# Kernel optimization log

Hardware: AMD Instinct MI355X
Metric: run time of the kernel (lower is better)

Reference implementation:

```python
import jax, jax.numpy as jnp
import numpy as np

B, S, H = 2, 2048, 2048
NH, NKV, HD = 32, 8, 64          # num_heads, num_kv_heads, head_dim
G = NH // NKV                     # GQA group size
NEG = -1e9


def setup_inputs() -> dict:
    key = jax.random.key(0)
    ks = jax.random.split(key, 8)
    x = jax.random.normal(ks[0], (B, S, H), dtype=jnp.float32)
    # real RoPE frequencies: theta = 10000 ** (-2i/hd)
    inv_freq = 1.0 / (10000.0 ** (np.arange(0, HD, 2, dtype=np.float32) / HD))
    angles = np.arange(S, dtype=np.float32)[:, None] * inv_freq[None, :]  # [S, HD//2]
    freqs_cos = jnp.asarray(np.cos(angles))
    freqs_sin = jnp.asarray(np.sin(angles))
    # additive causal mask [S, S]
    mask = jnp.where(jnp.tril(jnp.ones((S, S), dtype=bool)), 0.0, NEG).astype(jnp.float32)
    sc = 0.02
    Wq = jax.random.normal(ks[1], (NH * HD, H), dtype=jnp.float32) * sc
    bq = jax.random.normal(ks[2], (NH * HD,), dtype=jnp.float32) * sc
    Wk = jax.random.normal(ks[3], (NKV * HD, H), dtype=jnp.float32) * sc
    bk = jax.random.normal(ks[4], (NKV * HD,), dtype=jnp.float32) * sc
    Wv = jax.random.normal(ks[5], (NKV * HD, H), dtype=jnp.float32) * sc
    bv = jax.random.normal(ks[6], (NKV * HD,), dtype=jnp.float32) * sc
    Wo = jax.random.normal(ks[7], (H, NH * HD), dtype=jnp.float32) * sc
    return {"x": x, "freqs_cos": freqs_cos, "freqs_sin": freqs_sin, "mask": mask,
            "Wq": Wq, "bq": bq, "Wk": Wk, "bk": bk, "Wv": Wv, "bv": bv, "Wo": Wo}


def _rotate_half(t):
    h = t.shape[-1] // 2
    return jnp.concatenate([-t[..., h:], t[..., :h]], axis=-1)


def reference(x, freqs_cos, freqs_sin, mask, Wq, bq, Wk, bk, Wv, bv, Wo):
    b, s, _ = x.shape
    q = (x @ Wq.T + bq).reshape(b, s, NH, HD)
    k = (x @ Wk.T + bk).reshape(b, s, NKV, HD)
    v = (x @ Wv.T + bv).reshape(b, s, NKV, HD)
    # RoPE (rotate_half style): cos/sin duplicated along last dim -> [1, s, 1, HD]
    cos = jnp.concatenate([freqs_cos, freqs_cos], axis=-1)[None, :, None, :]
    sin = jnp.concatenate([freqs_sin, freqs_sin], axis=-1)[None, :, None, :]
    q = q * cos + _rotate_half(q) * sin
    k = k * cos + _rotate_half(k) * sin
    # GQA: view q as [b, s, NKV, G, HD]; avoids repeat_interleave of K/V (same math)
    q5 = q.reshape(b, s, NKV, G, HD)
    scores = jnp.einsum('bqhgd,bkhd->bhgqk', q5, k) / jnp.sqrt(jnp.float32(HD))
    scores = scores + mask  # broadcast [s, s] over [b, h, g, s, s]
    p = jax.nn.softmax(scores.astype(jnp.float32), axis=-1).astype(q.dtype)
    out = jnp.einsum('bhgqk,bkhd->bqhgd', p, v).reshape(b, s, NH * HD)
    return out @ Wo.T
```

## Files before the change

kernel.cpp:

```cpp
#include <hip/hip_runtime.h>
#include <hip/hip_bf16.h>
#include <cstddef>
#include <cstdint>

#define B_   2
#define S_   2048
#define H_   2048
#define NH_  32
#define NKV_ 8
#define HD_  64

typedef __attribute__((ext_vector_type(8))) short short8;
typedef __attribute__((ext_vector_type(4))) float v4f;
typedef __attribute__((ext_vector_type(16))) float v16f;

#define MAXC 48.0f
#define QSCALE 0.18033688011112042f

__device__ __forceinline__ unsigned short f2b(float f) {
    unsigned int u = __float_as_uint(f);
    u += 0x7FFFu + ((u >> 16) & 1u);
    return (unsigned short)(u >> 16);
}
__device__ __forceinline__ unsigned int pkbf(float a, float b) {
    __hip_bfloat162 h = __float22bfloat162_rn(float2{a, b});
    return *(unsigned int*)&h;
}
__device__ __forceinline__ v4f mfma16(short8 a, short8 b, v4f c) {
    return __builtin_amdgcn_mfma_f32_16x16x32_bf16(a, b, c, 0, 0, 0);
}
__device__ __forceinline__ v16f mfma32(short8 a, short8 b, v16f c) {
    return __builtin_amdgcn_mfma_f32_32x32x16_bf16(a, b, c, 0, 0, 0);
}
__device__ __forceinline__ void gll16(void* lds, const void* g) {
    __builtin_amdgcn_global_load_lds(
        (const __attribute__((address_space(1))) unsigned int*)g,
        (__attribute__((address_space(3))) unsigned int*)lds, 16, 0, 0);
}

__global__ __launch_bounds__(256) void convert_all(
    const float* __restrict__ x, const float* __restrict__ wq,
    const float* __restrict__ wk, const float* __restrict__ wv,
    const float* __restrict__ wo,
    unsigned short* __restrict__ xb, unsigned short* __restrict__ wqb,
    unsigned short* __restrict__ wkb, unsigned short* __restrict__ wvb,
    unsigned short* __restrict__ wob)
{
    size_t i = ((size_t)blockIdx.x * 256 + threadIdx.x) * 4;
    const float* src; unsigned short* dst; size_t off;
    if (i < 8388608)       { src = x;  dst = xb;  off = i; }
    else if (i < 12582912) { src = wq; dst = wqb; off = i - 8388608; }
    else if (i < 13631488) { src = wk; dst = wkb; off = i - 12582912; }
    else if (i < 14680064) { src = wv; dst = wvb; off = i - 13631488; }
    else                   { src = wo; dst = wob; off = i - 14680064; }
    float4 v = *(const float4*)(src + off);
    ushort4 o;
    o.x = f2b(v.x); o.y = f2b(v.y); o.z = f2b(v.z); o.w = f2b(v.w);
    *(ushort4*)(dst + off) = o;
}

__global__ __launch_bounds__(256) void qkv_gemm(
    const unsigned short* __restrict__ xb,
    const unsigned short* __restrict__ wqb, const unsigned short* __restrict__ wkb,
    const unsigned short* __restrict__ wvb,
    const float* __restrict__ bq, const float* __restrict__ bk,
    const float* __restrict__ bv,
    const float* __restrict__ fc, const float* __restrict__ fs,
    unsigned short* __restrict__ Qb, unsigned short* __restrict__ Kb,
    unsigned short* __restrict__ Vt)
{
    __shared__ unsigned short As[128 * 64];
    __shared__ unsigned short Bs[128 * 64];
    const int tid = threadIdx.x;
    const int lane = tid & 63, w = tid >> 6;
    const int tx = lane & 15, quad = lane >> 4;
    const int bx = blockIdx.x, by = blockIdx.y;

    const unsigned short *Ap, *Bp;
    int mode, aBase, bBase;
    if (bx < 16)      { mode = 0; Ap = xb;  Bp = wqb; aBase = by * 128; bBase = bx * 128; }
    else if (bx < 20) { mode = 1; Ap = xb;  Bp = wkb; aBase = by * 128; bBase = (bx - 16) * 128; }
    else              { mode = 2; Ap = wvb; Bp = xb;  aBase = (bx - 20) * 128; bBase = by * 128; }

    const int wm = (w >> 1) * 64, wn = (w & 1) * 64;
    v4f acc[4][4];
#pragma unroll
    for (int i = 0; i < 4; ++i)
#pragma unroll
        for (int j = 0; j < 4; ++j) acc[i][j] = (v4f)0.f;

    const int r8 = lane >> 3, gc = (lane & 7) ^ r8;
    const unsigned short* ga = &Ap[(size_t)(aBase + w * 32 + r8) * 2048 + gc * 8];
    const unsigned short* gb = &Bp[(size_t)(bBase + w * 32 + r8) * 2048 + gc * 8];

    const int t7 = tx & 7;
    int slA[2], slB[2];
#pragma unroll
    for (int kk = 0; kk < 2; ++kk) { slA[kk] = ((kk * 4 + quad) ^ t7) * 8; slB[kk] = slA[kk]; }

    for (int k0 = 0; k0 < 2048; k0 += 64) {
        __syncthreads();
#pragma unroll
        for (int i = 0; i < 4; ++i) {
            gll16(&As[(w * 32 + i * 8) * 64], ga + (size_t)(i * 8) * 2048 + k0);
            gll16(&Bs[(w * 32 + i * 8) * 64], gb + (size_t)(i * 8) * 2048 + k0);
        }
        __syncthreads();
#pragma unroll
        for (int kk = 0; kk < 2; ++kk) {
            short8 af[4], bf[4];
#pragma unroll
            for (int mt = 0; mt < 4; ++mt)
                af[mt] = *(const short8*)&As[(wm + mt * 16 + tx) * 64 + slA[kk]];
#pragma unroll
            for (int nt = 0; nt < 4; ++nt)
                bf[nt] = *(const short8*)&Bs[(wn + nt * 16 + tx) * 64 + slB[kk]];
#pragma unroll
            for (int mt = 0; mt < 4; ++mt)
#pragma unroll
                for (int nt = 0; nt < 4; ++nt)
                    acc[mt][nt] = mfma16(af[mt], bf[nt], acc[mt][nt]);
        }
    }

    if (mode <= 1) {
        unsigned short* Cout = mode ? Kb : Qb;
        const float* bias    = mode ? bk : bq;
        const int ldN        = mode ? 512 : 2048;
        const float scq      = mode ? 1.0f : QSCALE;
        float bx0 = bias[bBase + wn +  0 + tx];
        float bx1 = bias[bBase + wn + 16 + tx];
        float bx2 = bias[bBase + wn + 32 + tx];
        float bx3 = bias[bBase + wn + 48 + tx];
#pragma unroll
        for (int mt = 0; mt < 4; ++mt)
#pragma unroll
            for (int rg = 0; rg < 4; ++rg) {
                int m = aBase + wm + mt * 16 + quad * 4 + rg;
                int s = m & (S_ - 1);
                float c0 = fc[s * 32 + tx],      c1 = fc[s * 32 + 16 + tx];
                float s0 = fs[s * 32 + tx],      s1 = fs[s * 32 + 16 + tx];
                float q0 = acc[mt][0][rg] + bx0, q1 = acc[mt][1][rg] + bx1;
                float q2 = acc[mt][2][rg] + bx2, q3 = acc[mt][3][rg] + bx3;
                size_t base = (size_t)m * ldN + bBase + wn + tx;
                Cout[base]      = f2b((q0 * c0 - q2 * s0) * scq);
                Cout[base + 16] = f2b((q1 * c1 - q3 * s1) * scq);
                Cout[base + 32] = f2b((q2 * c0 + q0 * s0) * scq);
                Cout[base + 48] = f2b((q3 * c1 + q1 * s1) * scq);
            }
    } else {
#pragma unroll
        for (int mt = 0; mt < 4; ++mt)
#pragma unroll
            for (int rg = 0; rg < 4; ++rg) {
                int d = aBase + wm + mt * 16 + quad * 4 + rg;
                float bvv = bv[d];
                size_t base = (size_t)d * 4096 + bBase + wn + tx;
#pragma unroll
                for (int nt = 0; nt < 4; ++nt)
                    Vt[base + nt * 16] = f2b(acc[mt][nt][rg] + bvv);
            }
    }
}

__global__ __launch_bounds__(256) void out_gemm(
    const unsigned short* __restrict__ Ab, const unsigned short* __restrict__ Bw,
    float* __restrict__ C)
{
    __shared__ unsigned short As[128 * 64];
    __shared__ unsigned short Bs[128 * 64];
    const int tid = threadIdx.x;
    const int lane = tid & 63, w = tid >> 6;
    const int tx = lane & 15, quad = lane >> 4;
    const int bm = blockIdx.y * 128, bn = blockIdx.x * 128;
    const int wm = (w >> 1) * 64, wn = (w & 1) * 64;

    v4f acc[4][4];
#pragma unroll
    for (int i = 0; i < 4; ++i)
#pragma unroll
        for (int j = 0; j < 4; ++j) acc[i][j] = (v4f)0.f;

    const int r8 = lane >> 3, gc = (lane & 7) ^ r8;
    const unsigned short* ga = &Ab[(size_t)(bm + w * 32 + r8) * 2048 + gc * 8];
    const unsigned short* gb = &Bw[(size_t)(bn + w * 32 + r8) * 2048 + gc * 8];
    const int t7 = tx & 7;
    int sl[2];
#pragma unroll
    for (int kk = 0; kk < 2; ++kk) sl[kk] = ((kk * 4 + quad) ^ t7) * 8;

    for (int k0 = 0; k0 < 2048; k0 += 64) {
        __syncthreads();
#pragma unroll
        for (int i = 0; i < 4; ++i) {
            gll16(&As[(w * 32 + i * 8) * 64], ga + (size_t)(i * 8) * 2048 + k0);
            gll16(&Bs[(w * 32 + i * 8) * 64], gb + (size_t)(i * 8) * 2048 + k0);
        }
        __syncthreads();
#pragma unroll
        for (int kk = 0; kk < 2; ++kk) {
            short8 af[4], bf[4];
#pragma unroll
            for (int mt = 0; mt < 4; ++mt)
                af[mt] = *(const short8*)&As[(wm + mt * 16 + tx) * 64 + sl[kk]];
#pragma unroll
            for (int nt = 0; nt < 4; ++nt)
                bf[nt] = *(const short8*)&Bs[(wn + nt * 16 + tx) * 64 + sl[kk]];
#pragma unroll
            for (int mt = 0; mt < 4; ++mt)
#pragma unroll
                for (int nt = 0; nt < 4; ++nt)
                    acc[mt][nt] = mfma16(af[mt], bf[nt], acc[mt][nt]);
        }
    }
#pragma unroll
    for (int mt = 0; mt < 4; ++mt)
#pragma unroll
        for (int nt = 0; nt < 4; ++nt)
#pragma unroll
            for (int rg = 0; rg < 4; ++rg) {
                int m = bm + wm + mt * 16 + quad * 4 + rg;
                C[(size_t)m * 2048 + bn + wn + nt * 16 + tx] = acc[mt][nt][rg];
            }
}

__global__ __launch_bounds__(256) void attn_mfma(
    const unsigned short* __restrict__ Q, const unsigned short* __restrict__ K,
    const unsigned short* __restrict__ Vt, unsigned short* __restrict__ O)
{
    __shared__ __align__(16) unsigned short Ks[64 * 72];
    __shared__ __align__(16) unsigned short Vs[64 * 72];
    const int tid = threadIdx.x;
    const int lane = tid & 63, wq = tid >> 6;
    const int l32 = lane & 31, half = lane >> 5;
    const int p = blockIdx.x, h = blockIdx.y, b = blockIdx.z;
    const int kvh = h >> 2;
    const int qtw = (wq < 2) ? p : (31 - p);
    const int kt_hi = 31 - p;

    const int qrow = qtw * 64 + (wq & 1) * 32 + l32;
    const unsigned short* Qr = &Q[(((size_t)b * S_ + qrow) * NH_ + h) * HD_];
    short8 qf[4];
#pragma unroll
    for (int s = 0; s < 4; ++s)
        qf[s] = *(const short8*)(Qr + s * 16 + half * 8);

    float l = 0.f;
    v16f o0 = (v16f)0.f, o1 = (v16f)0.f;

    for (int kt = 0; kt <= kt_hi; ++kt) {
        __syncthreads();
#pragma unroll
        for (int i = 0; i < 2; ++i) {
            int e = tid + i * 256;
            int row = e >> 3, c8 = (e & 7) * 8;
            *(uint4*)&Ks[row * 72 + c8] =
                *(const uint4*)&K[(((size_t)b * S_ + kt * 64 + row) * NKV_ + kvh) * HD_ + c8];
            *(uint4*)&Vs[row * 72 + c8] =
                *(const uint4*)&Vt[(size_t)(kvh * 64 + row) * 4096 + b * 2048 + kt * 64 + c8];
        }
        __syncthreads();
        if (kt > qtw) continue;
        const bool diag = (kt == qtw);
        const int tpart = diag ? (wq & 1) : 2;

        for (int t = 0; t < 2; ++t) {
            if (diag && t > tpart) break;
            const int kb = (t * 32 + l32) * 72 + half * 8;
            v16f st = (v16f)(-MAXC);
            st = mfma32(*(const short8*)&Ks[kb],      qf[0], st);
            st = mfma32(*(const short8*)&Ks[kb + 16], qf[1], st);
            st = mfma32(*(const short8*)&Ks[kb + 32], qf[2], st);
            st = mfma32(*(const short8*)&Ks[kb + 48], qf[3], st);
            const bool part = diag && (t == tpart);
            float pv[16];
#pragma unroll
            for (int r = 0; r < 16; ++r) {
                int krow = (r & 3) + 8 * (r >> 2) + 4 * half;
                bool msk = part && (krow > l32);
                pv[r] = msk ? 0.f : exp2f(st[r]);
                l += pv[r];
            }
            unsigned int u[8];
#pragma unroll
            for (int g = 0; g < 4; ++g) {
                u[2 * g]     = pkbf(pv[4 * g],     pv[4 * g + 1]);
                u[2 * g + 1] = pkbf(pv[4 * g + 2], pv[4 * g + 3]);
            }
#pragma unroll
            for (int sg = 0; sg < 2; ++sg) {
                unsigned int a0 = u[4 * sg], a1 = u[4 * sg + 1];
                unsigned int b0 = u[4 * sg + 2], b1 = u[4 * sg + 3];
                unsigned int s0 = __shfl_xor((int)a0, 32);
                unsigned int s1 = __shfl_xor((int)a1, 32);
                unsigned int s2 = __shfl_xor((int)b0, 32);
                unsigned int s3 = __shfl_xor((int)b1, 32);
                uint4 fw;
                fw.x = half ? s2 : a0;
                fw.y = half ? s3 : a1;
                fw.z = half ? b0 : s0;
                fw.w = half ? b1 : s1;
                short8 pf = *(short8*)&fw;
                const int vo = (2 * t + sg) * 16 + half * 8;
                o0 = mfma32(*(const short8*)&Vs[l32 * 72 + vo],        pf, o0);
                o1 = mfma32(*(const short8*)&Vs[(32 + l32) * 72 + vo], pf, o1);
            }
        }
    }

    l += __shfl_xor(l, 32);
    float inv = 1.f / l;
    int qg = qtw * 64 + (wq & 1) * 32 + l32;
    unsigned short* orow = &O[((size_t)b * S_ + qg) * (NH_ * HD_) + h * HD_];
#pragma unroll
    for (int td = 0; td < 2; ++td) {
        const v16f& oo = td ? o1 : o0;
#pragma unroll
        for (int g = 0; g < 4; ++g) {
            int d = td * 32 + g * 8 + half * 4;
            uint2 uu;
            uu.x = pkbf(oo[4 * g] * inv,     oo[4 * g + 1] * inv);
            uu.y = pkbf(oo[4 * g + 2] * inv, oo[4 * g + 3] * inv);
            *(uint2*)&orow[d] = uu;
        }
    }
}

extern "C" void kernel_launch(void* const* d_in, const int* in_sizes, int n_in,
                              void* d_out, int out_size, void* d_ws, size_t ws_size,
                              hipStream_t stream)
{
    const float* x  = (const float*)d_in[0];
    const float* fc = (const float*)d_in[1];
    const float* fs = (const float*)d_in[2];
    const float* Wq = (const float*)d_in[4];
    const float* bq = (const float*)d_in[5];
    const float* Wk = (const float*)d_in[6];
    const float* bk = (const float*)d_in[7];
    const float* Wv = (const float*)d_in[8];
    const float* bv = (const float*)d_in[9];
    const float* Wo = (const float*)d_in[10];
    float* out = (float*)d_out;

    unsigned short* ws = (unsigned short*)d_ws;
    unsigned short* xb  = ws;
    unsigned short* wqb = ws + 8388608;
    unsigned short* wkb = ws + 12582912;
    unsigned short* wvb = ws + 13631488;
    unsigned short* wob = ws + 14680064;
    unsigned short* Qb  = ws + 18874368;
    unsigned short* Kb  = ws + 27262976;
    unsigned short* Vt  = ws + 29360128;
    unsigned short* Ob  = ws + 31457280;

    dim3 blk(256);
    convert_all<<<18432, blk, 0, stream>>>(x, Wq, Wk, Wv, Wo, xb, wqb, wkb, wvb, wob);
    qkv_gemm<<<dim3(24, 32), blk, 0, stream>>>(xb, wqb, wkb, wvb, bq, bk, bv,
                                               fc, fs, Qb, Kb, Vt);
    attn_mfma<<<dim3(16, NH_, B_), blk, 0, stream>>>(Qb, Kb, Vt, Ob);
    out_gemm<<<dim3(16, 32), blk, 0, stream>>>(Ob, wob, out);
}
```

Baseline: 371.8 us.

## Load attention K/V fragments directly from global memory instead of LDS staging

The attention kernel stops staging K and V tiles in shared memory with block-wide barriers. Each wave now reads its MFMA operands straight from global memory (through the caches) and loops only over its own causal range. This removes the __syncthreads calls and the waves that idled on tiles they did not need, and lets the two wave pairs run independently. The cost is strided, partly uncoalesced 16-byte global loads with higher latency and repeated reads of the same K/V data across waves. A small GEMM index cleanup is also included.

Measured after the change: 408.1 us. 9.8% more time.

```diff
diff --git a/kernel.cpp b/kernel.cpp
--- a/kernel.cpp
+++ b/kernel.cpp
@@ -94,9 +94,9 @@
     const unsigned short* gb = &Bp[(size_t)(bBase + w * 32 + r8) * 2048 + gc * 8];
 
     const int t7 = tx & 7;
-    int slA[2], slB[2];
-#pragma unroll
-    for (int kk = 0; kk < 2; ++kk) { slA[kk] = ((kk * 4 + quad) ^ t7) * 8; slB[kk] = slA[kk]; }
+    int sl[2];
+#pragma unroll
+    for (int kk = 0; kk < 2; ++kk) sl[kk] = ((kk * 4 + quad) ^ t7) * 8;
 
     for (int k0 = 0; k0 < 2048; k0 += 64) {
         __syncthreads();
@@ -111,10 +111,10 @@
             short8 af[4], bf[4];
 #pragma unroll
             for (int mt = 0; mt < 4; ++mt)
-                af[mt] = *(const short8*)&As[(wm + mt * 16 + tx) * 64 + slA[kk]];
+                af[mt] = *(const short8*)&As[(wm + mt * 16 + tx) * 64 + sl[kk]];
 #pragma unroll
             for (int nt = 0; nt < 4; ++nt)
-                bf[nt] = *(const short8*)&Bs[(wn + nt * 16 + tx) * 64 + slB[kk]];
+                bf[nt] = *(const short8*)&Bs[(wn + nt * 16 + tx) * 64 + sl[kk]];
 #pragma unroll
             for (int mt = 0; mt < 4; ++mt)
 #pragma unroll
@@ -228,15 +228,12 @@
     const unsigned short* __restrict__ Q, const unsigned short* __restrict__ K,
     const unsigned short* __restrict__ Vt, unsigned short* __restrict__ O)
 {
-    __shared__ __align__(16) unsigned short Ks[64 * 72];
-    __shared__ __align__(16) unsigned short Vs[64 * 72];
     const int tid = threadIdx.x;
     const int lane = tid & 63, wq = tid >> 6;
     const int l32 = lane & 31, half = lane >> 5;
     const int p = blockIdx.x, h = blockIdx.y, b = blockIdx.z;
     const int kvh = h >> 2;
     const int qtw = (wq < 2) ? p : (31 - p);
-    const int kt_hi = 31 - p;
 
     const int qrow = qtw * 64 + (wq & 1) * 32 + l32;
     const unsigned short* Qr = &Q[(((size_t)b * S_ + qrow) * NH_ + h) * HD_];
@@ -245,33 +242,28 @@
     for (int s = 0; s < 4; ++s)
         qf[s] = *(const short8*)(Qr + s * 16 + half * 8);
 
+    const unsigned short* Kr  = &K[(((size_t)b * S_ + l32) * NKV_ + kvh) * HD_ + half * 8];
+    const unsigned short* Vr0 = &Vt[(size_t)(kvh * 64 + l32) * 4096 + b * 2048 + half * 8];
+    const unsigned short* Vr1 = Vr0 + 32 * 4096;
+
     float l = 0.f;
     v16f o0 = (v16f)0.f, o1 = (v16f)0.f;
 
-    for (int kt = 0; kt <= kt_hi; ++kt) {
-        __syncthreads();
-#pragma unroll
-        for (int i = 0; i < 2; ++i) {
-            int e = tid + i * 256;
-            int row = e >> 3, c8 = (e & 7) * 8;
-            *(uint4*)&Ks[row * 72 + c8] =
-                *(const uint4*)&K[(((size_t)b * S_ + kt * 64 + row) * NKV_ + kvh) * HD_ + c8];
-            *(uint4*)&Vs[row * 72 + c8] =
-                *(const uint4*)&Vt[(size_t)(kvh * 64 + row) * 4096 + b * 2048 + kt * 64 + c8];
-        }
-        __syncthreads();
-        if (kt > qtw) continue;
+    for (int kt = 0; kt <= qtw; ++kt) {
         const bool diag = (kt == qtw);
         const int tpart = diag ? (wq & 1) : 2;
+        const unsigned short* Kt  = Kr + (size_t)kt * 64 * 512;
+        const unsigned short* Vk0 = Vr0 + kt * 64;
+        const unsigned short* Vk1 = Vr1 + kt * 64;
 
         for (int t = 0; t < 2; ++t) {
             if (diag && t > tpart) break;
-            const int kb = (t * 32 + l32) * 72 + half * 8;
+            const unsigned short* Ka = Kt + (size_t)t * 32 * 512;
             v16f st = (v16f)(-MAXC);
-            st = mfma32(*(const short8*)&Ks[kb],      qf[0], st);
-            st = mfma32(*(const short8*)&Ks[kb + 16], qf[1], st);
-            st = mfma32(*(const short8*)&Ks[kb + 32], qf[2], st);
-            st = mfma32(*(const short8*)&Ks[kb + 48], qf[3], st);
+            st = mfma32(*(const short8*)(Ka),      qf[0], st);
+            st = mfma32(*(const short8*)(Ka + 16), qf[1], st);
+            st = mfma32(*(const short8*)(Ka + 32), qf[2], st);
+            st = mfma32(*(const short8*)(Ka + 48), qf[3], st);
             const bool part = diag && (t == tpart);
             float pv[16];
 #pragma unroll
@@ -289,7 +281,7 @@
             }
 #pragma unroll
             for (int sg = 0; sg < 2; ++sg) {
-                unsigned int a0 = u[4 * sg], a1 = u[4 * sg + 1];
+                unsigned int a0 = u[4 * sg],     a1 = u[4 * sg + 1];
                 unsigned int b0 = u[4 * sg + 2], b1 = u[4 * sg + 3];
                 unsigned int s0 = __shfl_xor((int)a0, 32);
                 unsigned int s1 = __shfl_xor((int)a1, 32);
@@ -301,17 +293,16 @@
                 fw.z = half ? b0 : s0;
                 fw.w = half ? b1 : s1;
                 short8 pf = *(short8*)&fw;
-                const int vo = (2 * t + sg) * 16 + half * 8;
-                o0 = mfma32(*(const short8*)&Vs[l32 * 72 + vo],        pf, o0);
-                o1 = mfma32(*(const short8*)&Vs[(32 + l32) * 72 + vo], pf, o1);
+                const int vo = (2 * t + sg) * 16;
+                o0 = mfma32(*(const short8*)(Vk0 + vo), pf, o0);
+                o1 = mfma32(*(const short8*)(Vk1 + vo), pf, o1);
             }
         }
     }
 
     l += __shfl_xor(l, 32);
     float inv = 1.f / l;
-    int qg = qtw * 64 + (wq & 1) * 32 + l32;
-    unsigned short* orow = &O[((size_t)b * S_ + qg) * (NH_ * HD_) + h * HD_];
+    unsigned short* orow = &O[((size_t)b * S_ + qrow) * (NH_ * HD_) + h * HD_];
 #pragma unroll
     for (int td = 0; td < 2; ++td) {
         const v16f& oo = td ? o1 : o0;
```
